# Optimization experiments

Hardware: AMD Instinct MI355X
Metric: run time of the kernel (lower is better)

Reference implementation:

```python
import math
import jax, jax.numpy as jnp
import numpy as np

B, T, E = 2, 2048, 2048
H, HKV = 16, 4
DH = E // H              # 128
ROT_DIM = DH             # rotary_pct = 1.0 -> 128
ROT_HALF = ROT_DIM // 2  # RotaryEmbedding is built with dim=ROT_DIM//2=64; only these dims rotate
MAX_SEQ = 2048


def _rope_tables():
    # theta = 10000 ** (-arange(0, dim, 2)/dim) with dim = ROT_HALF
    theta = 10000.0 ** (-jnp.arange(0, ROT_HALF, 2, dtype=jnp.float32) / ROT_HALF)  # [ROT_HALF//2]
    pos = jnp.arange(MAX_SEQ, dtype=jnp.float32)
    angles = pos[:, None] * theta[None, :]   # [MAX_SEQ, ROT_HALF//2]
    return jnp.cos(angles), jnp.sin(angles)


def _apply_rotary(q, k, start_pos):
    # q: [B,T,H,ROT_DIM], k: [B,T,HKV,ROT_DIM]; rotate only first ROT_HALF dims (interleaved pairs)
    cos, sin = _rope_tables()
    t = q.shape[1]
    cos = jax.lax.dynamic_slice_in_dim(cos, start_pos, t, axis=0)[None, :, None, :]
    sin = jax.lax.dynamic_slice_in_dim(sin, start_pos, t, axis=0)[None, :, None, :]

    def rot(a):
        a_rot, a_pass = a[..., :ROT_HALF], a[..., ROT_HALF:]
        x, y = a_rot[..., 0::2], a_rot[..., 1::2]
        rx = x * cos - y * sin
        ry = x * sin + y * cos
        rotated = jnp.stack([rx, ry], axis=-1).reshape(*a_rot.shape)
        return jnp.concatenate([rotated, a_pass], axis=-1)

    return rot(q), rot(k)


def setup_inputs() -> dict:
    key = jax.random.key(0)
    ks = jax.random.split(key, 9)
    s = 0.02  # weight scale for sane logits
    return {
        "x": jax.random.normal(ks[0], (B, T, E), dtype=jnp.float32),
        "Wq": jax.random.normal(ks[1], (E, H * DH), dtype=jnp.float32) * s,
        "bq": jax.random.normal(ks[2], (H * DH,), dtype=jnp.float32) * s,
        "Wk": jax.random.normal(ks[3], (E, HKV * DH), dtype=jnp.float32) * s,
        "bk": jax.random.normal(ks[4], (HKV * DH,), dtype=jnp.float32) * s,
        "Wv": jax.random.normal(ks[5], (E, HKV * DH), dtype=jnp.float32) * s,
        "bv": jax.random.normal(ks[6], (HKV * DH,), dtype=jnp.float32) * s,
        "Wo": jax.random.normal(ks[7], (E, E), dtype=jnp.float32) * s,
        "bo": jax.random.normal(ks[8], (E,), dtype=jnp.float32) * s,
        "start_pos": 0,
    }


def reference(x, Wq, bq, Wk, bk, Wv, bv, Wo, bo, start_pos):
    b, t, _ = x.shape
    q = (x @ Wq + bq).reshape(b, t, H, DH)
    k = (x @ Wk + bk).reshape(b, t, HKV, DH)
    v = (x @ Wv + bv).reshape(b, t, HKV, DH)

    q, k = _apply_rotary(q, k, start_pos)

    group = H // HKV
    k = jnp.repeat(k, group, axis=2)  # [b,t,H,DH]
    v = jnp.repeat(v, group, axis=2)

    # scores: [b,H,t,t]
    scores = jnp.einsum("bqhd,bkhd->bhqk", q, k) / math.sqrt(DH)
    causal = jnp.tril(jnp.ones((t, t), dtype=bool))
    scores = jnp.where(causal[None, None], scores, -jnp.inf)
    probs = jax.nn.softmax(scores, axis=-1)

    out = jnp.einsum("bhqk,bkhd->bqhd", probs, v).reshape(b, t, H * DH)
    return out @ Wo + bo
```

## Files before the change

### kernel.cpp

```cpp
#include <hip/hip_runtime.h>

typedef __attribute__((ext_vector_type(8))) short short8;
typedef __attribute__((ext_vector_type(4))) float f32x4;
typedef __attribute__((ext_vector_type(16))) float f32x16;

#define DEVFN __device__ __forceinline__

DEVFN unsigned short f2bf(float f) {
  unsigned int u = __builtin_bit_cast(unsigned int, f);
  u += 0x7FFFu + ((u >> 16) & 1u);
  return (unsigned short)(u >> 16);
}
DEVFN float bf2f(unsigned int u) { return __builtin_bit_cast(float, u << 16); }

DEVFN unsigned int cvtpk_bf16(float lo, float hi) {
  unsigned int d;
  asm("v_cvt_pk_bf16_f32 %0, %1, %2" : "=v"(d) : "v"(lo), "v"(hi));
  return d;
}
DEVFN void plswap32(unsigned int& a, unsigned int& b) {
  asm("v_permlane32_swap_b32 %0, %1" : "+v"(a), "+v"(b));
}


__global__ __launch_bounds__(256) void mk_tables(float* __restrict__ cost, float* __restrict__ sint) {
  int gid = blockIdx.x * 256 + threadIdx.x;
  int pos = gid >> 5, i = gid & 31;
  float theta = powf(10000.0f, -(float)(2 * i) / 64.0f);
  float ang = (float)pos * theta;
  cost[gid] = cosf(ang);
  sint[gid] = sinf(ang);
}

__global__ __launch_bounds__(256) void bias_cat_k(const float* __restrict__ bq, const float* __restrict__ bk,
                                                  const float* __restrict__ bv, float* __restrict__ out) {
  int i = blockIdx.x * 256 + threadIdx.x;
  float v;
  if (i < 2048) v = bq[i];
  else if (i < 2560) v = bk[i - 2048];
  else v = bv[i - 2560];
  out[i] = v;
}

__global__ __launch_bounds__(256) void convx(const float* __restrict__ x, unsigned short* __restrict__ xb) {
  int gid = blockIdx.x * 256 + threadIdx.x;
  const float4* xv = (const float4*)x;
  float4 a = xv[(size_t)gid * 2], b = xv[(size_t)gid * 2 + 1];
  short8 u;
  u[0] = (short)f2bf(a.x); u[1] = (short)f2bf(a.y); u[2] = (short)f2bf(a.z); u[3] = (short)f2bf(a.w);
  u[4] = (short)f2bf(b.x); u[5] = (short)f2bf(b.y); u[6] = (short)f2bf(b.z); u[7] = (short)f2bf(b.w);
  *(short8*)(xb + (size_t)gid * 8) = u;
}

__global__ __launch_bounds__(256) void transw(const float* __restrict__ W, unsigned short* __restrict__ Wt, int ncols) {
  __shared__ float lds[32][33];
  int n0 = blockIdx.x * 32, k0 = blockIdx.y * 32;
  int tx = threadIdx.x & 31, ty = threadIdx.x >> 5;
  #pragma unroll
  for (int i = 0; i < 4; i++) {
    int kr = ty + i * 8;
    lds[kr][tx] = W[(size_t)(k0 + kr) * ncols + n0 + tx];
  }
  __syncthreads();
  #pragma unroll
  for (int i = 0; i < 4; i++) {
    int nr = ty + i * 8;
    Wt[(size_t)(n0 + nr) * 2048 + k0 + tx] = f2bf(lds[tx][nr]);
  }
}

template<int NH>
__global__ __launch_bounds__(256) void rope_scatter(const unsigned short* __restrict__ QKV,
    const float* __restrict__ cost, const float* __restrict__ sint, const int* __restrict__ spp,
    unsigned short* __restrict__ dst, int colOff, float scale) {
  constexpr int LOG2NH = (NH == 16) ? 4 : 2;
  int gid = blockIdx.x * 256 + threadIdx.x;
  int j = gid & 63;
  int h = (gid >> 6) & (NH - 1);
  int m = gid >> (6 + LOG2NH);
  int t = m & 2047;
  const unsigned short* src = QKV + (size_t)m * 3072 + colOff + h * 128 + 2 * j;
  unsigned int pair = *(const unsigned int*)src;
  float xv = bf2f(pair & 0xFFFFu), yv = bf2f(pair >> 16);
  float rx, ry;
  if (j < 32) {
    int pos = (spp[0] + t) & 2047;
    float c = cost[pos * 32 + j], s = sint[pos * 32 + j];
    rx = xv * c - yv * s;
    ry = xv * s + yv * c;
  } else { rx = xv; ry = yv; }
  rx *= scale; ry *= scale;
  size_t drow = ((size_t)((m >> 11) * NH + h)) * 2048 + t;
  unsigned int outp = (unsigned int)f2bf(rx) | ((unsigned int)f2bf(ry) << 16);
  *(unsigned int*)(dst + drow * 128 + 2 * j) = outp;
}

__global__ __launch_bounds__(256) void vtrans(const unsigned short* __restrict__ QKV, unsigned short* __restrict__ Vt) {
  __shared__ __align__(16) unsigned short lds[64 * 128];
  int tid = threadIdx.x;
  int t0 = blockIdx.x * 64;
  int bk = blockIdx.y;
  const unsigned short* src = QKV + (size_t)(bk >> 2) * 2048 * 3072 + 2560 + (bk & 3) * 128;
  #pragma unroll
  for (int c = 0; c < 4; c++) {
    int idx = c * 256 + tid;
    int tr = idx >> 4, dc = idx & 15;
    short8 v = *(const short8*)(src + (size_t)(t0 + tr) * 3072 + dc * 8);
    *(short8*)((char*)lds + tr * 256 + 16 * (dc ^ (tr >> 3))) = v;
  }
  __syncthreads();
  unsigned short* dstb = Vt + (size_t)bk * 128 * 2048;
  #pragma unroll
  for (int c2 = 0; c2 < 4; c2++) {
    int idx2 = c2 * 256 + tid;
    int tc = idx2 & 7, d = idx2 >> 3;
    short8 u;
    #pragma unroll
    for (int e = 0; e < 8; e++) {
      int t = 8 * tc + e;
      u[e] = *(const short*)((char*)lds + t * 256 + 16 * ((d >> 3) ^ tc) + (d & 7) * 2);
    }
    *(short8*)(dstb + (size_t)d * 2048 + t0 + 8 * tc) = u;
  }
}

template<bool BF16OUT>
__global__ __launch_bounds__(256, 2) void gemm_bt(
    const unsigned short* __restrict__ A, const unsigned short* __restrict__ Bt,
    const float* __restrict__ bias, void* __restrict__ Cout, int M, int N, int K) {
  __shared__ __align__(16) unsigned short Asl[128 * 64];
  __shared__ __align__(16) unsigned short Bsl[128 * 64];
  int tid = threadIdx.x;
  int lane = tid & 63, w = tid >> 6;
  int wr = w >> 1, wc = w & 1;
  int m0 = blockIdx.y * 128, n0 = blockIdx.x * 128;

  f32x4 acc[4][4];
  #pragma unroll
  for (int i = 0; i < 4; i++)
    #pragma unroll
    for (int j = 0; j < 4; j++)
      #pragma unroll
      for (int r = 0; r < 4; r++) acc[i][j][r] = 0.f;

  int srow = w * 32 + (lane >> 3);
  int kc8 = (lane & 7) * 8;
  const unsigned short* Aptr = A + (size_t)(m0 + srow) * K + kc8;
  const unsigned short* Bptr = Bt + (size_t)(n0 + srow) * K + kc8;
  unsigned short* AslW = Asl + w * 4 * 512;
  unsigned short* BslW = Bsl + w * 4 * 512;

  for (int k0 = 0; k0 < K; k0 += 64) {
    __syncthreads();
    #pragma unroll
    for (int i = 0; i < 4; i++) {
      __builtin_amdgcn_global_load_lds(
        (const __attribute__((address_space(1))) unsigned int*)(Aptr + (size_t)i * 8 * K + k0),
        (__attribute__((address_space(3))) unsigned int*)(AslW + i * 512), 16, 0, 0);
      __builtin_amdgcn_global_load_lds(
        (const __attribute__((address_space(1))) unsigned int*)(Bptr + (size_t)i * 8 * K + k0),
        (__attribute__((address_space(3))) unsigned int*)(BslW + i * 512), 16, 0, 0);
    }
    __syncthreads();
    #pragma unroll
    for (int ks = 0; ks < 2; ks++) {
      short8 af[4], bfr[4];
      #pragma unroll
      for (int mi = 0; mi < 4; mi++)
        af[mi] = *(const short8*)(Asl + (wr * 64 + mi * 16 + (lane & 15)) * 64 + ks * 32 + (lane >> 4) * 8);
      #pragma unroll
      for (int ni = 0; ni < 4; ni++)
        bfr[ni] = *(const short8*)(Bsl + (wc * 64 + ni * 16 + (lane & 15)) * 64 + ks * 32 + (lane >> 4) * 8);
      #pragma unroll
      for (int mi = 0; mi < 4; mi++)
        #pragma unroll
        for (int ni = 0; ni < 4; ni++)
          acc[mi][ni] = __builtin_amdgcn_mfma_f32_16x16x32_bf16(af[mi], bfr[ni], acc[mi][ni], 0, 0, 0);
    }
  }
  int cl = lane & 15, rq = lane >> 4;
  #pragma unroll
  for (int mi = 0; mi < 4; mi++) {
    #pragma unroll
    for (int ni = 0; ni < 4; ni++) {
      int gn = n0 + wc * 64 + ni * 16 + cl;
      float bv = bias[gn];
      #pragma unroll
      for (int r = 0; r < 4; r++) {
        int gm = m0 + wr * 64 + mi * 16 + rq * 4 + r;
        float v = acc[mi][ni][r] + bv;
        if (BF16OUT) ((unsigned short*)Cout)[(size_t)gm * N + gn] = f2bf(v);
        else ((float*)Cout)[(size_t)gm * N + gn] = v;
      }
    }
  }
}

__global__ __launch_bounds__(128, 2) void attn_kernel(
    const unsigned short* __restrict__ Qr, const unsigned short* __restrict__ Kr,
    const unsigned short* __restrict__ Vt, unsigned short* __restrict__ O) {
  __shared__ __align__(16) unsigned short K_lds[64 * 136];
  __shared__ __align__(16) unsigned short V_lds[128 * 72];
  __shared__ float bl_lds[2 * 32];

  const int tid = threadIdx.x;
  const int lane = tid & 63;
  const int w = tid >> 6;
  const int l31 = lane & 31;
  const int hf = lane >> 5;
  const int q0 = blockIdx.x * 64;
  const int bh = blockIdx.y;
  const int b = bh >> 4, h = bh & 15;
  const int kh = h >> 2;
  const int qw = q0 + w * 32;

  const unsigned short* qbase = Qr + (((size_t)(b * 16 + h)) * 2048 + (qw + l31)) * 128;
  short8 qf[8];
  #pragma unroll
  for (int s = 0; s < 8; s++)
    qf[s] = *(const short8*)(qbase + s * 16 + hf * 8);

  float m_r = -3.0e38f, l_r = 0.f;
  f32x16 oacc[4];
  #pragma unroll
  for (int dt = 0; dt < 4; dt++)
    #pragma unroll
    for (int r = 0; r < 16; r++) oacc[dt][r] = 0.f;

  const unsigned short* kbase = Kr + ((size_t)(b * 4 + kh)) * 2048 * 128;
  const unsigned short* vbase = Vt + ((size_t)(b * 4 + kh)) * 128 * 2048;

  const int ntiles = blockIdx.x + 1;
  for (int kt = 0; kt < ntiles; kt++) {
    const int kv0 = kt * 64;
    __syncthreads();
    #pragma unroll
    for (int c = 0; c < 8; c++) {
      int idx = c * 128 + tid;
      int kvr = idx >> 4, dc = idx & 15;
      short8 v = *(const short8*)(kbase + (size_t)(kv0 + kvr) * 128 + dc * 8);
      *(short8*)((char*)K_lds + kvr * 272 + dc * 16) = v;
    }
    #pragma unroll
    for (int c = 0; c < 8; c++) {
      int idx = c * 128 + tid;
      int d = idx >> 3, kvc = idx & 7;
      short8 v = *(const short8*)(vbase + (size_t)d * 2048 + kv0 + kvc * 8);
      *(short8*)((char*)V_lds + d * 144 + kvc * 16) = v;
    }
    __syncthreads();

    f32x16 sc[2];
    #pragma unroll
    for (int ct = 0; ct < 2; ct++) {
      #pragma unroll
      for (int r = 0; r < 16; r++) sc[ct][r] = 0.f;
      #pragma unroll
      for (int s = 0; s < 8; s++) {
        short8 kf = *(const short8*)((char*)K_lds + (ct * 32 + l31) * 272 + s * 32 + hf * 16);
        sc[ct] = __builtin_amdgcn_mfma_f32_32x32x16_bf16(kf, qf[s], sc[ct], 0, 0, 0);
      }
    }
    if (kv0 + 63 > qw) {
      #pragma unroll
      for (int ct = 0; ct < 2; ct++)
        #pragma unroll
        for (int r = 0; r < 16; r++) {
          int kg = kv0 + ct * 32 + (r & 3) + 8 * (r >> 2) + 4 * hf;
          if (kg > qw + l31) sc[ct][r] = -3.0e38f;
        }
    }
    float mx[16];
    #pragma unroll
    for (int r = 0; r < 16; r++) mx[r] = fmaxf(sc[0][r], sc[1][r]);
    #pragma unroll
    for (int s2 = 8; s2 >= 1; s2 >>= 1)
      #pragma unroll
      for (int i = 0; i < 8; i++) if (i < s2) mx[i] = fmaxf(mx[i], mx[i + s2]);
    float tm = fmaxf(mx[0], __shfl_xor(mx[0], 32));
    float mn = fmaxf(m_r, tm);
    float al = __builtin_amdgcn_exp2f(m_r - mn);
    m_r = mn;
    #pragma unroll
    for (int ct = 0; ct < 2; ct++)
      #pragma unroll
      for (int r = 0; r < 16; r++) sc[ct][r] = __builtin_amdgcn_exp2f(sc[ct][r] - mn);
    float sm[16];
    #pragma unroll
    for (int r = 0; r < 16; r++) sm[r] = sc[0][r] + sc[1][r];
    #pragma unroll
    for (int s2 = 8; s2 >= 1; s2 >>= 1)
      #pragma unroll
      for (int i = 0; i < 8; i++) if (i < s2) sm[i] += sm[i + s2];
    float rs = sm[0] + __shfl_xor(sm[0], 32);
    l_r = l_r * al + rs;
    if (lane < 32) bl_lds[w * 32 + l31] = al;

    short8 pa[4];
    #pragma unroll
    for (int ks = 0; ks < 4; ks++) {
      const int ct = ks >> 1, kb = (ks & 1) * 8;
      unsigned int A0 = cvtpk_bf16(sc[ct][kb + 0], sc[ct][kb + 1]);
      unsigned int A1 = cvtpk_bf16(sc[ct][kb + 2], sc[ct][kb + 3]);
      unsigned int B0 = cvtpk_bf16(sc[ct][kb + 4], sc[ct][kb + 5]);
      unsigned int B1 = cvtpk_bf16(sc[ct][kb + 6], sc[ct][kb + 7]);
      plswap32(A0, B0);
      plswap32(A1, B1);
      union { unsigned int wds[4]; short8 s8; } u;
      u.wds[0] = A0; u.wds[1] = A1; u.wds[2] = B0; u.wds[3] = B1;
      pa[ks] = u.s8;
    }
    #pragma unroll
    for (int r = 0; r < 16; r++) {
      float alr = bl_lds[w * 32 + (r & 3) + 8 * (r >> 2) + 4 * hf];
      #pragma unroll
      for (int dt = 0; dt < 4; dt++) oacc[dt][r] *= alr;
    }
    #pragma unroll
    for (int dt = 0; dt < 4; dt++) {
      #pragma unroll
      for (int ks = 0; ks < 4; ks++) {
        short8 vf = *(const short8*)((char*)V_lds + (dt * 32 + l31) * 144 + ks * 32 + hf * 16);
        oacc[dt] = __builtin_amdgcn_mfma_f32_32x32x16_bf16(pa[ks], vf, oacc[dt], 0, 0, 0);
      }
    }
  }
  if (lane < 32) bl_lds[w * 32 + l31] = 1.0f / l_r;
  #pragma unroll
  for (int r = 0; r < 16; r++) {
    int rloc = (r & 3) + 8 * (r >> 2) + 4 * hf;
    float inv = bl_lds[w * 32 + rloc];
    int qg = qw + rloc;
    unsigned short* orow = O + ((size_t)(b * 2048 + qg)) * 2048 + h * 128;
    #pragma unroll
    for (int dt = 0; dt < 4; dt++)
      orow[dt * 32 + l31] = f2bf(oacc[dt][r] * inv);
  }
}

extern "C" void kernel_launch(void* const* d_in, const int* in_sizes, int n_in,
                              void* d_out, int out_size, void* d_ws, size_t ws_size,
                              hipStream_t stream) {
  (void)in_sizes; (void)n_in; (void)out_size; (void)ws_size;
  const float* x  = (const float*)d_in[0];
  const float* Wq = (const float*)d_in[1];
  const float* bq = (const float*)d_in[2];
  const float* Wk = (const float*)d_in[3];
  const float* bk = (const float*)d_in[4];
  const float* Wv = (const float*)d_in[5];
  const float* bv = (const float*)d_in[6];
  const float* Wo = (const float*)d_in[7];
  const float* bo = (const float*)d_in[8];
  const int*   sp = (const int*)d_in[9];

  char* ws = (char*)d_ws;
  unsigned short* xb    = (unsigned short*)ws;
  unsigned short* Wqkvt = (unsigned short*)(ws + 16777216);
  unsigned short* Wot   = (unsigned short*)(ws + 29360128);
  unsigned short* QKVb  = (unsigned short*)(ws + 37748736);
  float* cost           = (float*)(ws + 62914560);
  float* sint           = (float*)(ws + 63176704);
  float* bcat           = (float*)(ws + 63438848);

  unsigned short* Obuf = xb;
  unsigned short* Qr = (unsigned short*)d_out;
  unsigned short* Kr = (unsigned short*)((char*)d_out + 16777216);
  unsigned short* Vtb = (unsigned short*)((char*)d_out + 20971520);

  mk_tables<<<256, 256, 0, stream>>>(cost, sint);
  bias_cat_k<<<12, 256, 0, stream>>>(bq, bk, bv, bcat);
  convx<<<4096, 256, 0, stream>>>(x, xb);
  transw<<<dim3(64, 64), 256, 0, stream>>>(Wq, Wqkvt, 2048);
  transw<<<dim3(16, 64), 256, 0, stream>>>(Wk, Wqkvt + (size_t)2048 * 2048, 512);
  transw<<<dim3(16, 64), 256, 0, stream>>>(Wv, Wqkvt + (size_t)2560 * 2048, 512);
  transw<<<dim3(64, 64), 256, 0, stream>>>(Wo, Wot, 2048);
  gemm_bt<true><<<dim3(24, 32), 256, 0, stream>>>(xb, Wqkvt, bcat, QKVb, 4096, 3072, 2048);
  rope_scatter<16><<<16384, 256, 0, stream>>>(QKVb, cost, sint, sp, Qr, 0, 0.12751743f);
  rope_scatter<4><<<4096, 256, 0, stream>>>(QKVb, cost, sint, sp, Kr, 2048, 1.0f);
  vtrans<<<dim3(32, 8), 256, 0, stream>>>(QKVb, Vtb);
  attn_kernel<<<dim3(32, 32), 128, 0, stream>>>(Qr, Kr, Vtb, Obuf);
  gemm_bt<false><<<dim3(16, 32), 256, 0, stream>>>(Obuf, Wot, bo, (float*)d_out, 4096, 2048, 2048);
}
```

Baseline: 256.3 us.

## Use single-wave attention blocks with direct global K/V loads and heavy-first scheduling

The attention kernel now launches one 64-thread wave per 32-row query tile on a flattened 2048-block grid. A swizzle interleaves batch/heads and orders the longest causal tiles first. K and V fragments are read straight from global memory into registers instead of being staged through LDS behind two block barriers. Per-row rescale factors are broadcast with ds_bpermute instead of an LDS array. This removes barrier and LDS round-trip costs and evens out the causal load imbalance, but each wave now fetches its own copy of K/V, which roughly doubles cache traffic and exposes global-load latency.

```diff
diff --git a/kernel.cpp b/kernel.cpp
--- a/kernel.cpp
+++ b/kernel.cpp
@@ -20,6 +20,10 @@
 }
 DEVFN void plswap32(unsigned int& a, unsigned int& b) {
   asm("v_permlane32_swap_b32 %0, %1" : "+v"(a), "+v"(b));
+}
+DEVFN float bcast32(float v, int srclane) {
+  int r = __builtin_amdgcn_ds_bpermute(srclane * 4, __builtin_bit_cast(int, v));
+  return __builtin_bit_cast(float, r);
 }
 
 
@@ -196,23 +200,19 @@
   }
 }
 
-__global__ __launch_bounds__(128, 2) void attn_kernel(
+__global__ __launch_bounds__(64) void attn_kernel(
     const unsigned short* __restrict__ Qr, const unsigned short* __restrict__ Kr,
     const unsigned short* __restrict__ Vt, unsigned short* __restrict__ O) {
-  __shared__ __align__(16) unsigned short K_lds[64 * 136];
-  __shared__ __align__(16) unsigned short V_lds[128 * 72];
-  __shared__ float bl_lds[2 * 32];
-
-  const int tid = threadIdx.x;
-  const int lane = tid & 63;
-  const int w = tid >> 6;
+  const int lane = threadIdx.x;
   const int l31 = lane & 31;
   const int hf = lane >> 5;
-  const int q0 = blockIdx.x * 64;
-  const int bh = blockIdx.y;
+  const int bid = blockIdx.x;
+  const int swz = (bid & 7) * 256 + (bid >> 3);
+  const int bh = swz >> 6;
+  const int qtile = 63 - (swz & 63);
   const int b = bh >> 4, h = bh & 15;
   const int kh = h >> 2;
-  const int qw = q0 + w * 32;
+  const int qw = qtile * 32;
 
   const unsigned short* qbase = Qr + (((size_t)(b * 16 + h)) * 2048 + (qw + l31)) * 128;
   short8 qf[8];
@@ -230,25 +230,9 @@
   const unsigned short* kbase = Kr + ((size_t)(b * 4 + kh)) * 2048 * 128;
   const unsigned short* vbase = Vt + ((size_t)(b * 4 + kh)) * 128 * 2048;
 
-  const int ntiles = blockIdx.x + 1;
+  const int ntiles = (qtile >> 1) + 1;
   for (int kt = 0; kt < ntiles; kt++) {
     const int kv0 = kt * 64;
-    __syncthreads();
-    #pragma unroll
-    for (int c = 0; c < 8; c++) {
-      int idx = c * 128 + tid;
-      int kvr = idx >> 4, dc = idx & 15;
-      short8 v = *(const short8*)(kbase + (size_t)(kv0 + kvr) * 128 + dc * 8);
-      *(short8*)((char*)K_lds + kvr * 272 + dc * 16) = v;
-    }
-    #pragma unroll
-    for (int c = 0; c < 8; c++) {
-      int idx = c * 128 + tid;
-      int d = idx >> 3, kvc = idx & 7;
-      short8 v = *(const short8*)(vbase + (size_t)d * 2048 + kv0 + kvc * 8);
-      *(short8*)((char*)V_lds + d * 144 + kvc * 16) = v;
-    }
-    __syncthreads();
 
     f32x16 sc[2];
     #pragma unroll
@@ -257,10 +241,18 @@
       for (int r = 0; r < 16; r++) sc[ct][r] = 0.f;
       #pragma unroll
       for (int s = 0; s < 8; s++) {
-        short8 kf = *(const short8*)((char*)K_lds + (ct * 32 + l31) * 272 + s * 32 + hf * 16);
+        short8 kf = *(const short8*)(kbase + (size_t)(kv0 + ct * 32 + l31) * 128 + s * 16 + hf * 8);
         sc[ct] = __builtin_amdgcn_mfma_f32_32x32x16_bf16(kf, qf[s], sc[ct], 0, 0, 0);
       }
     }
+
+    short8 vf[4][4];
+    #pragma unroll
+    for (int dt = 0; dt < 4; dt++)
+      #pragma unroll
+      for (int ks = 0; ks < 4; ks++)
+        vf[dt][ks] = *(const short8*)(vbase + (size_t)(dt * 32 + l31) * 2048 + kv0 + ks * 16 + hf * 8);
+
     if (kv0 + 63 > qw) {
       #pragma unroll
       for (int ct = 0; ct < 2; ct++)
@@ -294,7 +286,6 @@
       for (int i = 0; i < 8; i++) if (i < s2) sm[i] += sm[i + s2];
     float rs = sm[0] + __shfl_xor(sm[0], 32);
     l_r = l_r * al + rs;
-    if (lane < 32) bl_lds[w * 32 + l31] = al;
 
     short8 pa[4];
     #pragma unroll
@@ -312,24 +303,21 @@
     }
     #pragma unroll
     for (int r = 0; r < 16; r++) {
-      float alr = bl_lds[w * 32 + (r & 3) + 8 * (r >> 2) + 4 * hf];
+      float alr = bcast32(al, (r & 3) + 8 * (r >> 2) + 4 * hf);
       #pragma unroll
       for (int dt = 0; dt < 4; dt++) oacc[dt][r] *= alr;
     }
     #pragma unroll
-    for (int dt = 0; dt < 4; dt++) {
-      #pragma unroll
-      for (int ks = 0; ks < 4; ks++) {
-        short8 vf = *(const short8*)((char*)V_lds + (dt * 32 + l31) * 144 + ks * 32 + hf * 16);
-        oacc[dt] = __builtin_amdgcn_mfma_f32_32x32x16_bf16(pa[ks], vf, oacc[dt], 0, 0, 0);
-      }
-    }
-  }
-  if (lane < 32) bl_lds[w * 32 + l31] = 1.0f / l_r;
+    for (int dt = 0; dt < 4; dt++)
+      #pragma unroll
+      for (int ks = 0; ks < 4; ks++)
+        oacc[dt] = __builtin_amdgcn_mfma_f32_32x32x16_bf16(pa[ks], vf[dt][ks], oacc[dt], 0, 0, 0);
+  }
+  float invl = 1.0f / l_r;
   #pragma unroll
   for (int r = 0; r < 16; r++) {
     int rloc = (r & 3) + 8 * (r >> 2) + 4 * hf;
-    float inv = bl_lds[w * 32 + rloc];
+    float inv = bcast32(invl, rloc);
     int qg = qw + rloc;
     unsigned short* orow = O + ((size_t)(b * 2048 + qg)) * 2048 + h * 128;
     #pragma unroll
@@ -378,6 +366,6 @@
   rope_scatter<16><<<16384, 256, 0, stream>>>(QKVb, cost, sint, sp, Qr, 0, 0.12751743f);
   rope_scatter<4><<<4096, 256, 0, stream>>>(QKVb, cost, sint, sp, Kr, 2048, 1.0f);
   vtrans<<<dim3(32, 8), 256, 0, stream>>>(QKVb, Vtb);
-  attn_kernel<<<dim3(32, 32), 128, 0, stream>>>(Qr, Kr, Vtb, Obuf);
+  attn_kernel<<<dim3(2048), 64, 0, stream>>>(Qr, Kr, Vtb, Obuf);
   gemm_bt<false><<<dim3(16, 32), 256, 0, stream>>>(Obuf, Wot, bo, (float*)d_out, 4096, 2048, 2048);
 }
```

New measurement: 313.1 us. 22.2% more time.

## Balance causal attention by pairing q-tiles, prefetch KV via registers, lazy rescale

Applied to the files above, without the earlier changes.

The attention kernel now uses 256-thread blocks of four waves. Two waves take early query tiles and two take mirrored late tiles, so every block does about the same causal work, and blocks are launched as a flat 512-block grid. The next K/V tile is loaded into registers while the current one is computed, overlapping global loads with MFMA work. Online softmax rescaling is skipped unless the running max grows by more than a threshold, the row sum is kept per half-wave, and LDS broadcasts are replaced with ds_bpermute. The costs are higher register pressure and waves idling through barriers on tiles they do not need.

```diff
diff --git a/kernel.cpp b/kernel.cpp
--- a/kernel.cpp
+++ b/kernel.cpp
@@ -20,6 +20,10 @@
 }
 DEVFN void plswap32(unsigned int& a, unsigned int& b) {
   asm("v_permlane32_swap_b32 %0, %1" : "+v"(a), "+v"(b));
+}
+DEVFN float bcast32(float v, int srclane) {
+  int r = __builtin_amdgcn_ds_bpermute(srclane * 4, __builtin_bit_cast(int, v));
+  return __builtin_bit_cast(float, r);
 }
 
 
@@ -196,23 +200,26 @@
   }
 }
 
-__global__ __launch_bounds__(128, 2) void attn_kernel(
+__global__ __launch_bounds__(256) void attn_kernel(
     const unsigned short* __restrict__ Qr, const unsigned short* __restrict__ Kr,
     const unsigned short* __restrict__ Vt, unsigned short* __restrict__ O) {
   __shared__ __align__(16) unsigned short K_lds[64 * 136];
   __shared__ __align__(16) unsigned short V_lds[128 * 72];
-  __shared__ float bl_lds[2 * 32];
 
   const int tid = threadIdx.x;
   const int lane = tid & 63;
   const int w = tid >> 6;
   const int l31 = lane & 31;
   const int hf = lane >> 5;
-  const int q0 = blockIdx.x * 64;
-  const int bh = blockIdx.y;
+  const int dctl = blockIdx.x;
+  const int bx = dctl >> 5;
+  const int bh = dctl & 31;
   const int b = bh >> 4, h = bh & 15;
   const int kh = h >> 2;
-  const int qw = q0 + w * 32;
+  const int qt = (w < 2) ? (2 * bx + w) : (60 - 2 * bx + w);
+  const int qw = qt * 32;
+  const int nw = (qt >> 1) + 1;
+  const int nbt = 32 - bx;
 
   const unsigned short* qbase = Qr + (((size_t)(b * 16 + h)) * 2048 + (qw + l31)) * 128;
   short8 qf[8];
@@ -230,106 +237,119 @@
   const unsigned short* kbase = Kr + ((size_t)(b * 4 + kh)) * 2048 * 128;
   const unsigned short* vbase = Vt + ((size_t)(b * 4 + kh)) * 128 * 2048;
 
-  const int ntiles = blockIdx.x + 1;
-  for (int kt = 0; kt < ntiles; kt++) {
+  int krow[4], kcol[4], vdr[4], vkc[4];
+  #pragma unroll
+  for (int c = 0; c < 4; c++) {
+    int idx = c * 256 + tid;
+    krow[c] = idx >> 4; kcol[c] = idx & 15;
+    vdr[c] = idx >> 3;  vkc[c] = idx & 7;
+  }
+  short8 kreg[4], vreg[4];
+  #pragma unroll
+  for (int c = 0; c < 4; c++) {
+    kreg[c] = *(const short8*)(kbase + (size_t)krow[c] * 128 + kcol[c] * 8);
+    vreg[c] = *(const short8*)(vbase + (size_t)vdr[c] * 2048 + vkc[c] * 8);
+  }
+
+  for (int kt = 0; kt < nbt; kt++) {
     const int kv0 = kt * 64;
     __syncthreads();
     #pragma unroll
-    for (int c = 0; c < 8; c++) {
-      int idx = c * 128 + tid;
-      int kvr = idx >> 4, dc = idx & 15;
-      short8 v = *(const short8*)(kbase + (size_t)(kv0 + kvr) * 128 + dc * 8);
-      *(short8*)((char*)K_lds + kvr * 272 + dc * 16) = v;
-    }
-    #pragma unroll
-    for (int c = 0; c < 8; c++) {
-      int idx = c * 128 + tid;
-      int d = idx >> 3, kvc = idx & 7;
-      short8 v = *(const short8*)(vbase + (size_t)d * 2048 + kv0 + kvc * 8);
-      *(short8*)((char*)V_lds + d * 144 + kvc * 16) = v;
+    for (int c = 0; c < 4; c++) {
+      *(short8*)((char*)K_lds + krow[c] * 272 + kcol[c] * 16) = kreg[c];
+      *(short8*)((char*)V_lds + vdr[c] * 144 + vkc[c] * 16) = vreg[c];
     }
     __syncthreads();
-
-    f32x16 sc[2];
-    #pragma unroll
-    for (int ct = 0; ct < 2; ct++) {
-      #pragma unroll
-      for (int r = 0; r < 16; r++) sc[ct][r] = 0.f;
-      #pragma unroll
-      for (int s = 0; s < 8; s++) {
-        short8 kf = *(const short8*)((char*)K_lds + (ct * 32 + l31) * 272 + s * 32 + hf * 16);
-        sc[ct] = __builtin_amdgcn_mfma_f32_32x32x16_bf16(kf, qf[s], sc[ct], 0, 0, 0);
-      }
-    }
-    if (kv0 + 63 > qw) {
+    if (kt + 1 < nbt) {
+      const int kn = kv0 + 64;
+      #pragma unroll
+      for (int c = 0; c < 4; c++) {
+        kreg[c] = *(const short8*)(kbase + (size_t)(kn + krow[c]) * 128 + kcol[c] * 8);
+        vreg[c] = *(const short8*)(vbase + (size_t)vdr[c] * 2048 + kn + vkc[c] * 8);
+      }
+    }
+    if (kt < nw) {
+      f32x16 sc[2];
+      #pragma unroll
+      for (int ct = 0; ct < 2; ct++) {
+        #pragma unroll
+        for (int r = 0; r < 16; r++) sc[ct][r] = 0.f;
+        #pragma unroll
+        for (int s = 0; s < 8; s++) {
+          short8 kf = *(const short8*)((char*)K_lds + (ct * 32 + l31) * 272 + s * 32 + hf * 16);
+          sc[ct] = __builtin_amdgcn_mfma_f32_32x32x16_bf16(kf, qf[s], sc[ct], 0, 0, 0);
+        }
+      }
+      if (kv0 + 63 > qw) {
+        #pragma unroll
+        for (int ct = 0; ct < 2; ct++)
+          #pragma unroll
+          for (int r = 0; r < 16; r++) {
+            int kg = kv0 + ct * 32 + (r & 3) + 8 * (r >> 2) + 4 * hf;
+            if (kg > qw + l31) sc[ct][r] = -3.0e38f;
+          }
+      }
+      float mx[16];
+      #pragma unroll
+      for (int r = 0; r < 16; r++) mx[r] = fmaxf(sc[0][r], sc[1][r]);
+      #pragma unroll
+      for (int s2 = 8; s2 >= 1; s2 >>= 1)
+        #pragma unroll
+        for (int i = 0; i < 8; i++) if (i < s2) mx[i] = fmaxf(mx[i], mx[i + s2]);
+      float tm = fmaxf(mx[0], __shfl_xor(mx[0], 32));
+      if (__any(tm > m_r + 8.0f)) {
+        float mn = fmaxf(m_r, tm);
+        float al = __builtin_amdgcn_exp2f(m_r - mn);
+        m_r = mn;
+        l_r *= al;
+        #pragma unroll
+        for (int r = 0; r < 16; r++) {
+          float alr = bcast32(al, (r & 3) + 8 * (r >> 2) + 4 * hf);
+          #pragma unroll
+          for (int dt = 0; dt < 4; dt++) oacc[dt][r] *= alr;
+        }
+      }
       #pragma unroll
       for (int ct = 0; ct < 2; ct++)
         #pragma unroll
-        for (int r = 0; r < 16; r++) {
-          int kg = kv0 + ct * 32 + (r & 3) + 8 * (r >> 2) + 4 * hf;
-          if (kg > qw + l31) sc[ct][r] = -3.0e38f;
+        for (int r = 0; r < 16; r++) sc[ct][r] = __builtin_amdgcn_exp2f(sc[ct][r] - m_r);
+      float sm[16];
+      #pragma unroll
+      for (int r = 0; r < 16; r++) sm[r] = sc[0][r] + sc[1][r];
+      #pragma unroll
+      for (int s2 = 8; s2 >= 1; s2 >>= 1)
+        #pragma unroll
+        for (int i = 0; i < 8; i++) if (i < s2) sm[i] += sm[i + s2];
+      l_r += sm[0];
+
+      short8 pa[4];
+      #pragma unroll
+      for (int ks = 0; ks < 4; ks++) {
+        const int ct = ks >> 1, kb = (ks & 1) * 8;
+        unsigned int A0 = cvtpk_bf16(sc[ct][kb + 0], sc[ct][kb + 1]);
+        unsigned int A1 = cvtpk_bf16(sc[ct][kb + 2], sc[ct][kb + 3]);
+        unsigned int B0 = cvtpk_bf16(sc[ct][kb + 4], sc[ct][kb + 5]);
+        unsigned int B1 = cvtpk_bf16(sc[ct][kb + 6], sc[ct][kb + 7]);
+        plswap32(A0, B0);
+        plswap32(A1, B1);
+        union { unsigned int wds[4]; short8 s8; } u;
+        u.wds[0] = A0; u.wds[1] = A1; u.wds[2] = B0; u.wds[3] = B1;
+        pa[ks] = u.s8;
+      }
+      #pragma unroll
+      for (int dt = 0; dt < 4; dt++)
+        #pragma unroll
+        for (int ks = 0; ks < 4; ks++) {
+          short8 vf = *(const short8*)((char*)V_lds + (dt * 32 + l31) * 144 + ks * 32 + hf * 16);
+          oacc[dt] = __builtin_amdgcn_mfma_f32_32x32x16_bf16(pa[ks], vf, oacc[dt], 0, 0, 0);
         }
     }
-    float mx[16];
-    #pragma unroll
-    for (int r = 0; r < 16; r++) mx[r] = fmaxf(sc[0][r], sc[1][r]);
-    #pragma unroll
-    for (int s2 = 8; s2 >= 1; s2 >>= 1)
-      #pragma unroll
-      for (int i = 0; i < 8; i++) if (i < s2) mx[i] = fmaxf(mx[i], mx[i + s2]);
-    float tm = fmaxf(mx[0], __shfl_xor(mx[0], 32));
-    float mn = fmaxf(m_r, tm);
-    float al = __builtin_amdgcn_exp2f(m_r - mn);
-    m_r = mn;
-    #pragma unroll
-    for (int ct = 0; ct < 2; ct++)
-      #pragma unroll
-      for (int r = 0; r < 16; r++) sc[ct][r] = __builtin_amdgcn_exp2f(sc[ct][r] - mn);
-    float sm[16];
-    #pragma unroll
-    for (int r = 0; r < 16; r++) sm[r] = sc[0][r] + sc[1][r];
-    #pragma unroll
-    for (int s2 = 8; s2 >= 1; s2 >>= 1)
-      #pragma unroll
-      for (int i = 0; i < 8; i++) if (i < s2) sm[i] += sm[i + s2];
-    float rs = sm[0] + __shfl_xor(sm[0], 32);
-    l_r = l_r * al + rs;
-    if (lane < 32) bl_lds[w * 32 + l31] = al;
-
-    short8 pa[4];
-    #pragma unroll
-    for (int ks = 0; ks < 4; ks++) {
-      const int ct = ks >> 1, kb = (ks & 1) * 8;
-      unsigned int A0 = cvtpk_bf16(sc[ct][kb + 0], sc[ct][kb + 1]);
-      unsigned int A1 = cvtpk_bf16(sc[ct][kb + 2], sc[ct][kb + 3]);
-      unsigned int B0 = cvtpk_bf16(sc[ct][kb + 4], sc[ct][kb + 5]);
-      unsigned int B1 = cvtpk_bf16(sc[ct][kb + 6], sc[ct][kb + 7]);
-      plswap32(A0, B0);
-      plswap32(A1, B1);
-      union { unsigned int wds[4]; short8 s8; } u;
-      u.wds[0] = A0; u.wds[1] = A1; u.wds[2] = B0; u.wds[3] = B1;
-      pa[ks] = u.s8;
-    }
-    #pragma unroll
-    for (int r = 0; r < 16; r++) {
-      float alr = bl_lds[w * 32 + (r & 3) + 8 * (r >> 2) + 4 * hf];
-      #pragma unroll
-      for (int dt = 0; dt < 4; dt++) oacc[dt][r] *= alr;
-    }
-    #pragma unroll
-    for (int dt = 0; dt < 4; dt++) {
-      #pragma unroll
-      for (int ks = 0; ks < 4; ks++) {
-        short8 vf = *(const short8*)((char*)V_lds + (dt * 32 + l31) * 144 + ks * 32 + hf * 16);
-        oacc[dt] = __builtin_amdgcn_mfma_f32_32x32x16_bf16(pa[ks], vf, oacc[dt], 0, 0, 0);
-      }
-    }
-  }
-  if (lane < 32) bl_lds[w * 32 + l31] = 1.0f / l_r;
+  }
+  float invl = 1.0f / (l_r + __shfl_xor(l_r, 32));
   #pragma unroll
   for (int r = 0; r < 16; r++) {
     int rloc = (r & 3) + 8 * (r >> 2) + 4 * hf;
-    float inv = bl_lds[w * 32 + rloc];
+    float inv = bcast32(invl, rloc);
     int qg = qw + rloc;
     unsigned short* orow = O + ((size_t)(b * 2048 + qg)) * 2048 + h * 128;
     #pragma unroll
@@ -378,6 +398,6 @@
   rope_scatter<16><<<16384, 256, 0, stream>>>(QKVb, cost, sint, sp, Qr, 0, 0.12751743f);
   rope_scatter<4><<<4096, 256, 0, stream>>>(QKVb, cost, sint, sp, Kr, 2048, 1.0f);
   vtrans<<<dim3(32, 8), 256, 0, stream>>>(QKVb, Vtb);
-  attn_kernel<<<dim3(32, 32), 128, 0, stream>>>(Qr, Kr, Vtb, Obuf);
+  attn_kernel<<<dim3(512), 256, 0, stream>>>(Qr, Kr, Vtb, Obuf);
   gemm_bt<false><<<dim3(16, 32), 256, 0, stream>>>(Obuf, Wot, bo, (float*)d_out, 4096, 2048, 2048);
 }
```

Result: no change. 256.2 us (-0.0%).
